# Optimization experiments

Measured on AMD Instinct MI355X. Metric: run time of the kernel, lower is better.

Reference implementation:

```python
import jax, jax.numpy as jnp
import numpy as np

B, C_IMG, H, W = 16, 512, 32, 32
C_AUD, K_LEN, N_HEADS = 512, 256, 8
HEAD_DIM = C_AUD // N_HEADS
EPS = 1e-5


def setup_inputs() -> dict:
    key = jax.random.key(0)
    ks = jax.random.split(key, 12)
    s_img = 1.0 / np.sqrt(C_IMG)
    s_aud = 1.0 / np.sqrt(C_AUD)
    return {
        "img_feat": jax.random.normal(ks[0], (B, C_IMG, H, W), jnp.float32),
        "audio_feat": jax.random.normal(ks[1], (B, K_LEN, C_AUD), jnp.float32),
        "Wq": jax.random.uniform(ks[2], (C_IMG, C_AUD), jnp.float32, -s_img, s_img),
        "bq": jnp.zeros((C_AUD,), jnp.float32),
        "Wk": jax.random.uniform(ks[3], (C_AUD, C_AUD), jnp.float32, -s_aud, s_aud),
        "bk": jnp.zeros((C_AUD,), jnp.float32),
        "Wv": jax.random.uniform(ks[4], (C_AUD, C_AUD), jnp.float32, -s_aud, s_aud),
        "bv": jnp.zeros((C_AUD,), jnp.float32),
        "Wo": jax.random.uniform(ks[5], (C_AUD, C_IMG), jnp.float32, -s_aud, s_aud),
        "bo": jnp.zeros((C_IMG,), jnp.float32),
        "gamma": jnp.ones((C_IMG,), jnp.float32),
        "beta": jnp.zeros((C_IMG,), jnp.float32),
    }


def reference(img_feat, audio_feat, Wq, bq, Wk, bk, Wv, bv, Wo, bo, gamma, beta):
    b, c, h, w = img_feat.shape
    # b c h w -> b (h w) c
    img_seq = img_feat.reshape(b, c, h * w).transpose(0, 2, 1)
    q = img_seq @ Wq + bq                      # [b, q, C_AUD]
    k = audio_feat @ Wk + bk                   # [b, k, C_AUD]
    v = audio_feat @ Wv + bv
    # split heads: b s (h d) -> b h s d
    def split(x):
        bs, s, _ = x.shape
        return x.reshape(bs, s, N_HEADS, HEAD_DIM).transpose(0, 2, 1, 3)
    qh, kh, vh = split(q), split(k), split(v)
    scale = HEAD_DIM ** -0.5
    scores = jnp.einsum('bhqd,bhkd->bhqk', qh, kh) * scale
    weights = jax.nn.softmax(scores, axis=-1)
    attn = jnp.einsum('bhqk,bhkd->bhqd', weights, vh)
    attn = attn.transpose(0, 2, 1, 3).reshape(b, h * w, C_AUD)
    proj = attn @ Wo + bo                      # [b, q, C_IMG]
    y = img_seq + proj
    mu = jnp.mean(y, axis=-1, keepdims=True)
    var = jnp.mean((y - mu) ** 2, axis=-1, keepdims=True)
    y = (y - mu) * jax.lax.rsqrt(var + EPS) * gamma + beta
    # b (h w) c -> b c h w
    return y.transpose(0, 2, 1).reshape(b, c, h, w)
```

## Files before the change

### kernel.cpp

```cpp
#include <hip/hip_runtime.h>
#include <cstddef>

#define B_SZ 16
#define HW 1024
#define CCH 512
#define K_LEN 256
#define N_HEADS 8
#define EPS 1e-5f

typedef __bf16 bf16;
typedef bf16 bf16x8 __attribute__((ext_vector_type(8)));
typedef bf16 bf16x4 __attribute__((ext_vector_type(4)));
typedef float f32x4 __attribute__((ext_vector_type(4)));

__device__ __forceinline__ void gl_lds16(const bf16* g, bf16* l) {
    __builtin_amdgcn_global_load_lds(
        (const __attribute__((address_space(1))) void*)g,
        (__attribute__((address_space(3))) void*)l, 16, 0, 0);
}

__global__ __launch_bounds__(256) void transpose_cast_img(
    const float* __restrict__ src, bf16* __restrict__ dst)
{
    const int b  = blockIdx.z;
    const int s0 = blockIdx.x * 64;
    const int c0 = blockIdx.y * 64;
    __shared__ bf16 T[64][72];
    const int tid = threadIdx.x;
    {
        const int r = tid >> 2, cs = (tid & 3) << 4;
        const float* sp = src + ((size_t)b * CCH + c0 + r) * HW + s0 + cs;
        #pragma unroll
        for (int i = 0; i < 4; ++i) {
            float4 f = *(const float4*)(sp + i * 4);
            T[r][cs + i*4 + 0] = (bf16)f.x;
            T[r][cs + i*4 + 1] = (bf16)f.y;
            T[r][cs + i*4 + 2] = (bf16)f.z;
            T[r][cs + i*4 + 3] = (bf16)f.w;
        }
    }
    __syncthreads();
    {
        const int ss = tid >> 2, ks = (tid & 3) << 4;
        bf16x8 a, b8;
        #pragma unroll
        for (int j = 0; j < 8; ++j) { a[j] = T[ks + j][ss]; b8[j] = T[ks + 8 + j][ss]; }
        bf16* dp = dst + ((size_t)b * HW + s0 + ss) * CCH + c0 + ks;
        *(bf16x8*)dp = a;
        *(bf16x8*)(dp + 8) = b8;
    }
}

__global__ __launch_bounds__(256) void transpose_cast_w(
    const float* __restrict__ Wq, const float* __restrict__ Wk,
    const float* __restrict__ Wv, const float* __restrict__ Wo,
    bf16* __restrict__ dst)
{
    const int w = blockIdx.z;
    const float* src = (w == 0) ? Wq : (w == 1) ? Wk : (w == 2) ? Wv : Wo;
    const int n0 = blockIdx.x * 64;
    const int k0 = blockIdx.y * 64;
    __shared__ bf16 T[64][72];
    const int tid = threadIdx.x;
    {
        const int r = tid >> 2, cs = (tid & 3) << 4;
        const float* sp = src + (size_t)(k0 + r) * CCH + n0 + cs;
        #pragma unroll
        for (int i = 0; i < 4; ++i) {
            float4 f = *(const float4*)(sp + i * 4);
            T[r][cs + i*4 + 0] = (bf16)f.x;
            T[r][cs + i*4 + 1] = (bf16)f.y;
            T[r][cs + i*4 + 2] = (bf16)f.z;
            T[r][cs + i*4 + 3] = (bf16)f.w;
        }
    }
    __syncthreads();
    {
        const int nn = tid >> 2, ks = (tid & 3) << 4;
        bf16x8 a, b8;
        #pragma unroll
        for (int j = 0; j < 8; ++j) { a[j] = T[ks + j][nn]; b8[j] = T[ks + 8 + j][nn]; }
        bf16* dp = dst + (size_t)w * CCH * CCH + (size_t)(n0 + nn) * CCH + k0 + ks;
        *(bf16x8*)dp = a;
        *(bf16x8*)(dp + 8) = b8;
    }
}

__global__ __launch_bounds__(256) void cast_audio(
    const float* __restrict__ src, bf16* __restrict__ dst)
{
    const size_t i = ((size_t)blockIdx.x * 256 + threadIdx.x) * 8;
    float4 a = *(const float4*)(src + i);
    float4 b = *(const float4*)(src + i + 4);
    bf16x8 o;
    o[0] = (bf16)a.x; o[1] = (bf16)a.y; o[2] = (bf16)a.z; o[3] = (bf16)a.w;
    o[4] = (bf16)b.x; o[5] = (bf16)b.y; o[6] = (bf16)b.z; o[7] = (bf16)b.w;
    *(bf16x8*)(dst + i) = o;
}

__global__ __launch_bounds__(256) void gemm_bf16_mfma(
    const bf16* __restrict__ A, const bf16* __restrict__ Bt,
    const float* __restrict__ bias, bf16* __restrict__ out)
{
    const int tid  = threadIdx.x;
    const int wave = tid >> 6, lane = tid & 63;
    const int m0 = blockIdx.x * 128;
    const int n0 = blockIdx.y * 128;
    const int l15 = lane & 15, quad = lane >> 4;
    const int wm = (wave >> 1) * 64, wn = (wave & 1) * 64;

    __shared__ bf16 As[128 * 32];
    __shared__ bf16 Bs[128 * 32];

    const int r16 = lane >> 2;
    const int ks  = (lane & 3) * 8;

    f32x4 acc[4][4];
    #pragma unroll
    for (int i = 0; i < 4; ++i)
        #pragma unroll
        for (int j = 0; j < 4; ++j)
            acc[i][j] = (f32x4){0.f, 0.f, 0.f, 0.f};

    for (int k0 = 0; k0 < 512; k0 += 32) {
        #pragma unroll
        for (int i = 0; i < 2; ++i) {
            const int c = wave * 2 + i;
            gl_lds16(A  + (size_t)(m0 + c * 16 + r16) * 512 + k0 + ks, &As[c * 512]);
            gl_lds16(Bt + (size_t)(n0 + c * 16 + r16) * 512 + k0 + ks, &Bs[c * 512]);
        }
        __syncthreads();
        bf16x8 af[4], bfr[4];
        #pragma unroll
        for (int i = 0; i < 4; ++i)
            af[i] = *(const bf16x8*)&As[(wm + i * 16 + l15) * 32 + quad * 8];
        #pragma unroll
        for (int j = 0; j < 4; ++j)
            bfr[j] = *(const bf16x8*)&Bs[(wn + j * 16 + l15) * 32 + quad * 8];
        #pragma unroll
        for (int i = 0; i < 4; ++i)
            #pragma unroll
            for (int j = 0; j < 4; ++j)
                acc[i][j] = __builtin_amdgcn_mfma_f32_16x16x32_bf16(bfr[j], af[i], acc[i][j], 0, 0, 0);
        __syncthreads();
    }

    #pragma unroll
    for (int j = 0; j < 4; ++j) {
        const int gn = n0 + wn + j * 16 + quad * 4;
        const float4 bv4 = *(const float4*)(bias + gn);
        const float bb[4] = {bv4.x, bv4.y, bv4.z, bv4.w};
        #pragma unroll
        for (int i = 0; i < 4; ++i) {
            const int gm = m0 + wm + i * 16 + l15;
            bf16x4 ov;
            #pragma unroll
            for (int r = 0; r < 4; ++r) ov[r] = (bf16)(acc[i][j][r] + bb[r]);
            *(bf16x4*)(out + (size_t)gm * 512 + gn) = ov;
        }
    }
}

__global__ __launch_bounds__(256) void gemm_kv_mfma(
    const bf16* __restrict__ A, const bf16* __restrict__ Bt,
    const float* __restrict__ bk, const float* __restrict__ bv,
    bf16* __restrict__ khout, bf16* __restrict__ vtout)
{
    const int tid  = threadIdx.x;
    const int wave = tid >> 6, lane = tid & 63;
    const int m0 = blockIdx.x * 128;
    const int n0 = blockIdx.y * 128;
    const int l15 = lane & 15, quad = lane >> 4;
    const int wm = (wave >> 1) * 64, wn = (wave & 1) * 64;

    __shared__ bf16 As[128 * 32];
    __shared__ bf16 Bs[128 * 32];

    const int r16 = lane >> 2;
    const int ks  = (lane & 3) * 8;

    f32x4 acc[4][4];
    #pragma unroll
    for (int i = 0; i < 4; ++i)
        #pragma unroll
        for (int j = 0; j < 4; ++j)
            acc[i][j] = (f32x4){0.f, 0.f, 0.f, 0.f};

    for (int k0 = 0; k0 < 512; k0 += 32) {
        #pragma unroll
        for (int i = 0; i < 2; ++i) {
            const int c = wave * 2 + i;
            gl_lds16(A  + (size_t)(m0 + c * 16 + r16) * 512 + k0 + ks, &As[c * 512]);
            gl_lds16(Bt + (size_t)(n0 + c * 16 + r16) * 512 + k0 + ks, &Bs[c * 512]);
        }
        __syncthreads();
        bf16x8 af[4], bfr[4];
        #pragma unroll
        for (int i = 0; i < 4; ++i)
            af[i] = *(const bf16x8*)&As[(wm + i * 16 + l15) * 32 + quad * 8];
        #pragma unroll
        for (int j = 0; j < 4; ++j)
            bfr[j] = *(const bf16x8*)&Bs[(wn + j * 16 + l15) * 32 + quad * 8];
        #pragma unroll
        for (int i = 0; i < 4; ++i)
            #pragma unroll
            for (int j = 0; j < 4; ++j)
                acc[i][j] = __builtin_amdgcn_mfma_f32_16x16x32_bf16(af[i], bfr[j], acc[i][j], 0, 0, 0);
        __syncthreads();
    }

    #pragma unroll
    for (int j = 0; j < 4; ++j) {
        const int gn = n0 + wn + j * 16 + l15;
        if (gn < 512) {
            const int h = gn >> 6, d = gn & 63;
            const float bias = bk[gn];
            #pragma unroll
            for (int i = 0; i < 4; ++i) {
                const int gm = m0 + wm + i * 16 + quad * 4;
                const int b = gm >> 8, key = gm & 255;
                bf16* base = khout + ((((size_t)b * N_HEADS + h) * K_LEN) + key) * 64 + d;
                #pragma unroll
                for (int r = 0; r < 4; ++r)
                    base[(size_t)r * 64] = (bf16)(acc[i][j][r] + bias);
            }
        } else {
            const int ch = gn - 512;
            const int h = ch >> 6, d = ch & 63;
            const float bias = bv[ch];
            #pragma unroll
            for (int i = 0; i < 4; ++i) {
                const int gm = m0 + wm + i * 16 + quad * 4;
                const int b = gm >> 8, key = gm & 255;
                bf16x4 pk;
                #pragma unroll
                for (int r = 0; r < 4; ++r) pk[r] = (bf16)(acc[i][j][r] + bias);
                *(bf16x4*)(vtout + (((size_t)b * N_HEADS + h) * 64 + d) * K_LEN + key) = pk;
            }
        }
    }
}

__global__ __launch_bounds__(256) void attn_mfma(
    const bf16* __restrict__ q,
    const bf16* __restrict__ kh,
    const bf16* __restrict__ vt,
    bf16* __restrict__ o)
{
    const int bh = blockIdx.x;
    const int s0 = blockIdx.y * 64;
    const int tid = threadIdx.x;
    const int wave = tid >> 6, lane = tid & 63;
    const int l15 = lane & 15, quad = lane >> 4;
    const int b = bh >> 3, h = bh & 7;

    __shared__ bf16 KsPt[18432];
    __shared__ bf16 Vs[16896];

    const bf16* khb = kh + (size_t)bh * K_LEN * 64;
    const bf16* vtb = vt + (size_t)bh * 64 * K_LEN;

    #pragma unroll
    for (int i = 0; i < 8; ++i) {
        const int chunk = tid + (i << 8);
        const int key = chunk >> 3, dseg = (chunk & 7) << 3;
        *(bf16x8*)&KsPt[key * 72 + dseg] = *(const bf16x8*)(khb + key * 64 + dseg);
        const int d = chunk >> 5, kseg = (chunk & 31) << 3;
        *(bf16x8*)&Vs[d * 264 + kseg] = *(const bf16x8*)(vtb + d * 256 + kseg);
    }
    __syncthreads();

    const int qrow = s0 + wave * 16 + l15;
    const bf16* qp = q + ((size_t)(b * HW + qrow)) * 512 + h * 64 + quad * 8;
    const bf16x8 qf0 = *(const bf16x8*)qp;
    const bf16x8 qf1 = *(const bf16x8*)(qp + 32);

    f32x4 acc[16];
    #pragma unroll
    for (int m = 0; m < 16; ++m) acc[m] = (f32x4){0.f, 0.f, 0.f, 0.f};
    #pragma unroll
    for (int m = 0; m < 16; ++m) {
        const bf16x8 a0 = *(const bf16x8*)&KsPt[(m * 16 + l15) * 72 + quad * 8];
        const bf16x8 a1 = *(const bf16x8*)&KsPt[(m * 16 + l15) * 72 + 32 + quad * 8];
        acc[m] = __builtin_amdgcn_mfma_f32_16x16x32_bf16(a0, qf0, acc[m], 0, 0, 0);
        acc[m] = __builtin_amdgcn_mfma_f32_16x16x32_bf16(a1, qf1, acc[m], 0, 0, 0);
    }

    float mx = -1e30f;
    #pragma unroll
    for (int m = 0; m < 16; ++m)
        mx = fmaxf(mx, fmaxf(fmaxf(acc[m][0], acc[m][1]), fmaxf(acc[m][2], acc[m][3])));
    mx = fmaxf(mx, __shfl_xor(mx, 16, 64));
    mx = fmaxf(mx, __shfl_xor(mx, 32, 64));

    __syncthreads();

    bf16* PtW = &KsPt[wave * 4224];
    float l_sum = 0.f;
    #pragma unroll
    for (int m = 0; m < 16; ++m) {
        bf16x4 pk;
        #pragma unroll
        for (int r = 0; r < 4; ++r) {
            const float p = __expf((acc[m][r] - mx) * 0.125f);
            l_sum += p;
            pk[r] = (bf16)p;
        }
        *(bf16x4*)&PtW[l15 * 264 + m * 16 + quad * 4] = pk;
    }
    l_sum += __shfl_xor(l_sum, 16, 64);
    l_sum += __shfl_xor(l_sum, 32, 64);
    __syncthreads();

    f32x4 oacc[4];
    #pragma unroll
    for (int m = 0; m < 4; ++m) oacc[m] = (f32x4){0.f, 0.f, 0.f, 0.f};
    #pragma unroll
    for (int s = 0; s < 8; ++s) {
        const bf16x8 pb = *(const bf16x8*)&PtW[l15 * 264 + s * 32 + quad * 8];
        #pragma unroll
        for (int m = 0; m < 4; ++m) {
            const bf16x8 va = *(const bf16x8*)&Vs[(m * 16 + l15) * 264 + s * 32 + quad * 8];
            oacc[m] = __builtin_amdgcn_mfma_f32_16x16x32_bf16(va, pb, oacc[m], 0, 0, 0);
        }
    }

    const float inv = 1.0f / l_sum;
    bf16* op = o + ((size_t)(b * HW + qrow)) * 512 + h * 64 + quad * 4;
    #pragma unroll
    for (int m = 0; m < 4; ++m) {
        bf16x4 ov;
        #pragma unroll
        for (int r = 0; r < 4; ++r) ov[r] = (bf16)(oacc[m][r] * inv);
        *(bf16x4*)&op[m * 16] = ov;
    }
}

__global__ __launch_bounds__(256) void ln_kernel(
    const bf16* __restrict__ proj, const bf16* __restrict__ imgb,
    const float* __restrict__ gamma, const float* __restrict__ beta,
    float* __restrict__ out)
{
    const int b  = blockIdx.y;
    const int s0 = blockIdx.x * 32;
    const int tid = threadIdx.x;
    const int wave = tid >> 6, lane = tid & 63;

    __shared__ float Y[32][513];

    const int cb = lane * 8;
    const float4 g0 = *(const float4*)(gamma + cb);
    const float4 g1 = *(const float4*)(gamma + cb + 4);
    const float4 b0 = *(const float4*)(beta + cb);
    const float4 b1 = *(const float4*)(beta + cb + 4);
    const float gg[8] = {g0.x, g0.y, g0.z, g0.w, g1.x, g1.y, g1.z, g1.w};
    const float bb[8] = {b0.x, b0.y, b0.z, b0.w, b1.x, b1.y, b1.z, b1.w};

    #pragma unroll
    for (int rr = 0; rr < 8; ++rr) {
        const int ss = wave * 8 + rr;
        const size_t row = (size_t)b * HW + s0 + ss;
        bf16x8 p8 = *(const bf16x8*)(proj + row * 512 + cb);
        bf16x8 i8 = *(const bf16x8*)(imgb + row * 512 + cb);
        float y[8];
        float sum = 0.f, sq = 0.f;
        #pragma unroll
        for (int j = 0; j < 8; ++j) {
            y[j] = (float)p8[j] + (float)i8[j];
            sum += y[j]; sq += y[j] * y[j];
        }
        #pragma unroll
        for (int off = 32; off > 0; off >>= 1) {
            sum += __shfl_xor(sum, off, 64);
            sq  += __shfl_xor(sq, off, 64);
        }
        const float mu = sum * (1.f / 512.f);
        const float rs = rsqrtf(sq * (1.f / 512.f) - mu * mu + EPS);
        #pragma unroll
        for (int j = 0; j < 8; ++j)
            Y[ss][cb + j] = (y[j] - mu) * rs * gg[j] + bb[j];
    }
    __syncthreads();

    #pragma unroll
    for (int it = 0; it < 16; ++it) {
        const int idx = it * 256 + tid;
        const int c = idx >> 3, sseg = (idx & 7) << 2;
        float4 o4;
        o4.x = Y[sseg + 0][c];
        o4.y = Y[sseg + 1][c];
        o4.z = Y[sseg + 2][c];
        o4.w = Y[sseg + 3][c];
        *(float4*)(out + ((size_t)b * CCH + c) * HW + s0 + sseg) = o4;
    }
}

extern "C" void kernel_launch(void* const* d_in, const int* in_sizes, int n_in,
                              void* d_out, int out_size, void* d_ws, size_t ws_size,
                              hipStream_t stream) {
    const float* img   = (const float*)d_in[0];
    const float* audio = (const float*)d_in[1];
    const float* Wq    = (const float*)d_in[2];
    const float* bq    = (const float*)d_in[3];
    const float* Wk    = (const float*)d_in[4];
    const float* bk    = (const float*)d_in[5];
    const float* Wv    = (const float*)d_in[6];
    const float* bv    = (const float*)d_in[7];
    const float* Wo    = (const float*)d_in[8];
    const float* bo    = (const float*)d_in[9];
    const float* gamma = (const float*)d_in[10];
    const float* beta  = (const float*)d_in[11];

    bf16* wsb    = (bf16*)d_ws;
    bf16* img_bf = wsb;
    bf16* aud_bf = img_bf + 8388608;
    bf16* wT     = aud_bf + 2097152;
    bf16* q_bf   = wT + 1048576;
    bf16* kh_bf  = q_bf + 8388608;
    bf16* vt_bf  = kh_bf + 2097152;
    bf16* a_bf   = vt_bf + 2097152;
    bf16* p_bf   = q_bf;

    transpose_cast_img<<<dim3(16, 8, 16), 256, 0, stream>>>(img, img_bf);
    cast_audio<<<dim3(1024), 256, 0, stream>>>(audio, aud_bf);
    transpose_cast_w<<<dim3(8, 8, 4), 256, 0, stream>>>(Wq, Wk, Wv, Wo, wT);

    gemm_bf16_mfma<<<dim3(128, 4), 256, 0, stream>>>(img_bf, wT, bq, q_bf);
    gemm_kv_mfma<<<dim3(32, 8), 256, 0, stream>>>(aud_bf, wT + 262144, bk, bv, kh_bf, vt_bf);
    attn_mfma<<<dim3(B_SZ * N_HEADS, HW / 64), 256, 0, stream>>>(q_bf, kh_bf, vt_bf, a_bf);
    gemm_bf16_mfma<<<dim3(128, 4), 256, 0, stream>>>(a_bf, wT + 3 * 262144, bo, p_bf);
    ln_kernel<<<dim3(32, 16), 256, 0, stream>>>(p_bf, img_bf, gamma, beta, (float*)d_out);
}
```

Baseline: 198.1 us.

## Fuse output projection GEMM with residual add and LayerNorm epilogue

```diff
diff --git a/kernel.cpp b/kernel.cpp
--- a/kernel.cpp
+++ b/kernel.cpp
@@ -11,6 +11,7 @@
 typedef __bf16 bf16;
 typedef bf16 bf16x8 __attribute__((ext_vector_type(8)));
 typedef bf16 bf16x4 __attribute__((ext_vector_type(4)));
+typedef bf16 bf16x2 __attribute__((ext_vector_type(2)));
 typedef float f32x4 __attribute__((ext_vector_type(4)));
 
 __device__ __forceinline__ void gl_lds16(const bf16* g, bf16* l) {
@@ -148,14 +149,13 @@
     #pragma unroll
     for (int j = 0; j < 4; ++j) {
         const int gn = n0 + wn + j * 16 + quad * 4;
-        const float4 bv4 = *(const float4*)(bias + gn);
-        const float bb[4] = {bv4.x, bv4.y, bv4.z, bv4.w};
+        const f32x4 bv4 = *(const f32x4*)(bias + gn);
         #pragma unroll
         for (int i = 0; i < 4; ++i) {
             const int gm = m0 + wm + i * 16 + l15;
             bf16x4 ov;
             #pragma unroll
-            for (int r = 0; r < 4; ++r) ov[r] = (bf16)(acc[i][j][r] + bb[r]);
+            for (int r = 0; r < 4; ++r) ov[r] = (bf16)(acc[i][j][r] + bv4[r]);
             *(bf16x4*)(out + (size_t)gm * 512 + gn) = ov;
         }
     }
@@ -336,62 +336,136 @@
     }
 }
 
-__global__ __launch_bounds__(256) void ln_kernel(
-    const bf16* __restrict__ proj, const bf16* __restrict__ imgb,
+__global__ __launch_bounds__(512) void gemm_oln(
+    const bf16* __restrict__ A,
+    const bf16* __restrict__ Wt,
+    const float* __restrict__ bo,
+    const bf16* __restrict__ imgb,
     const float* __restrict__ gamma, const float* __restrict__ beta,
     float* __restrict__ out)
 {
-    const int b  = blockIdx.y;
-    const int s0 = blockIdx.x * 32;
-    const int tid = threadIdx.x;
+    const int tid  = threadIdx.x;
     const int wave = tid >> 6, lane = tid & 63;
-
-    __shared__ float Y[32][513];
-
-    const int cb = lane * 8;
-    const float4 g0 = *(const float4*)(gamma + cb);
-    const float4 g1 = *(const float4*)(gamma + cb + 4);
-    const float4 b0 = *(const float4*)(beta + cb);
-    const float4 b1 = *(const float4*)(beta + cb + 4);
-    const float gg[8] = {g0.x, g0.y, g0.z, g0.w, g1.x, g1.y, g1.z, g1.w};
-    const float bb[8] = {b0.x, b0.y, b0.z, b0.w, b1.x, b1.y, b1.z, b1.w};
-
-    #pragma unroll
-    for (int rr = 0; rr < 8; ++rr) {
-        const int ss = wave * 8 + rr;
-        const size_t row = (size_t)b * HW + s0 + ss;
-        bf16x8 p8 = *(const bf16x8*)(proj + row * 512 + cb);
-        bf16x8 i8 = *(const bf16x8*)(imgb + row * 512 + cb);
-        float y[8];
-        float sum = 0.f, sq = 0.f;
-        #pragma unroll
-        for (int j = 0; j < 8; ++j) {
-            y[j] = (float)p8[j] + (float)i8[j];
-            sum += y[j]; sq += y[j] * y[j];
-        }
-        #pragma unroll
-        for (int off = 32; off > 0; off >>= 1) {
-            sum += __shfl_xor(sum, off, 64);
-            sq  += __shfl_xor(sq, off, 64);
-        }
-        const float mu = sum * (1.f / 512.f);
-        const float rs = rsqrtf(sq * (1.f / 512.f) - mu * mu + EPS);
-        #pragma unroll
-        for (int j = 0; j < 8; ++j)
-            Y[ss][cb + j] = (y[j] - mu) * rs * gg[j] + bb[j];
-    }
-    __syncthreads();
-
-    #pragma unroll
-    for (int it = 0; it < 16; ++it) {
-        const int idx = it * 256 + tid;
-        const int c = idx >> 3, sseg = (idx & 7) << 2;
-        float4 o4;
-        o4.x = Y[sseg + 0][c];
-        o4.y = Y[sseg + 1][c];
-        o4.z = Y[sseg + 2][c];
-        o4.w = Y[sseg + 3][c];
-        *(float4*)(out + ((size_t)b * CCH + c) * HW + s0 + sseg) = o4;
+    const int l15 = lane & 15, quad = lane >> 4;
+    const int m0 = blockIdx.x * 64;
+    const int b  = m0 >> 10, s0 = m0 & 1023;
+    const int wn = wave * 64;
+
+    __shared__ union {
+        struct { bf16 As[64 * 32]; bf16 Bs[512 * 32]; } st;
+        bf16 Ys[64 * 522];
+    } u;
+    __shared__ float rsumS[64 * 8];
+    __shared__ float rsqS[64 * 8];
+
+    const int r16 = lane >> 2;
+    const int ks  = (lane & 3) * 8;
+
+    f32x4 acc[4][4];
+    #pragma unroll
+    for (int i = 0; i < 4; ++i)
+        #pragma unroll
+        for (int j = 0; j < 4; ++j)
+            acc[i][j] = (f32x4){0.f, 0.f, 0.f, 0.f};
+
+    for (int k0 = 0; k0 < 512; k0 += 32) {
+        #pragma unroll
+        for (int t = 0; t < 4; ++t) {
+            const int cb = wave + (t << 3);
+            gl_lds16(Wt + (size_t)(cb * 16 + r16) * 512 + k0 + ks, &u.st.Bs[cb * 512]);
+        }
+        if (wave < 4)
+            gl_lds16(A + (size_t)(m0 + wave * 16 + r16) * 512 + k0 + ks, &u.st.As[wave * 512]);
+        __syncthreads();
+        bf16x8 af[4], bfr[4];
+        #pragma unroll
+        for (int i = 0; i < 4; ++i)
+            af[i] = *(const bf16x8*)&u.st.As[(i * 16 + l15) * 32 + quad * 8];
+        #pragma unroll
+        for (int j = 0; j < 4; ++j)
+            bfr[j] = *(const bf16x8*)&u.st.Bs[(wn + j * 16 + l15) * 32 + quad * 8];
+        #pragma unroll
+        for (int i = 0; i < 4; ++i)
+            #pragma unroll
+            for (int j = 0; j < 4; ++j)
+                acc[i][j] = __builtin_amdgcn_mfma_f32_16x16x32_bf16(bfr[j], af[i], acc[i][j], 0, 0, 0);
+        __syncthreads();
+    }
+
+    float rs_[4] = {0.f, 0.f, 0.f, 0.f};
+    float rq_[4] = {0.f, 0.f, 0.f, 0.f};
+    #pragma unroll
+    for (int j = 0; j < 4; ++j) {
+        const int n = wn + j * 16 + quad * 4;
+        const f32x4 bo4 = *(const f32x4*)(bo + n);
+        #pragma unroll
+        for (int i = 0; i < 4; ++i) {
+            const int lm = i * 16 + l15;
+            const bf16x4 res = *(const bf16x4*)(imgb + (size_t)(m0 + lm) * 512 + n);
+            #pragma unroll
+            for (int r = 0; r < 4; ++r) {
+                const float y = acc[i][j][r] + bo4[r] + (float)res[r];
+                acc[i][j][r] = y;
+                rs_[i] += y;
+                rq_[i] += y * y;
+            }
+        }
+    }
+    #pragma unroll
+    for (int i = 0; i < 4; ++i) {
+        rs_[i] += __shfl_xor(rs_[i], 16, 64);
+        rs_[i] += __shfl_xor(rs_[i], 32, 64);
+        rq_[i] += __shfl_xor(rq_[i], 16, 64);
+        rq_[i] += __shfl_xor(rq_[i], 32, 64);
+    }
+    if (quad == 0) {
+        #pragma unroll
+        for (int i = 0; i < 4; ++i) {
+            rsumS[(i * 16 + l15) * 8 + wave] = rs_[i];
+            rsqS[(i * 16 + l15) * 8 + wave]  = rq_[i];
+        }
+    }
+    __syncthreads();
+
+    float mu[4], rstd[4];
+    #pragma unroll
+    for (int i = 0; i < 4; ++i) {
+        const int lm = i * 16 + l15;
+        float s = 0.f, q = 0.f;
+        #pragma unroll
+        for (int w = 0; w < 8; ++w) { s += rsumS[lm * 8 + w]; q += rsqS[lm * 8 + w]; }
+        mu[i] = s * (1.f / 512.f);
+        rstd[i] = rsqrtf(q * (1.f / 512.f) - mu[i] * mu[i] + EPS);
+    }
+
+    #pragma unroll
+    for (int j = 0; j < 4; ++j) {
+        const int n = wn + j * 16 + quad * 4;
+        const f32x4 g4 = *(const f32x4*)(gamma + n);
+        const f32x4 b4 = *(const f32x4*)(beta + n);
+        #pragma unroll
+        for (int i = 0; i < 4; ++i) {
+            const int lm = i * 16 + l15;
+            float z[4];
+            #pragma unroll
+            for (int r = 0; r < 4; ++r)
+                z[r] = (acc[i][j][r] - mu[i]) * rstd[i] * g4[r] + b4[r];
+            bf16x2 z01, z23;
+            z01[0] = (bf16)z[0]; z01[1] = (bf16)z[1];
+            z23[0] = (bf16)z[2]; z23[1] = (bf16)z[3];
+            *(bf16x2*)&u.Ys[lm * 522 + n]     = z01;
+            *(bf16x2*)&u.Ys[lm * 522 + n + 2] = z23;
+        }
+    }
+    __syncthreads();
+
+    float* ob = out + (size_t)b * CCH * HW + s0 + lane;
+    #pragma unroll
+    for (int it = 0; it < 32; ++it) {
+        const int c = wn + it * 2;
+        const bf16x2 z2 = *(const bf16x2*)&u.Ys[lane * 522 + c];
+        ob[(size_t)c * HW]       = (float)z2[0];
+        ob[(size_t)(c + 1) * HW] = (float)z2[1];
     }
 }
 
@@ -419,7 +493,6 @@
     bf16* kh_bf  = q_bf + 8388608;
     bf16* vt_bf  = kh_bf + 2097152;
     bf16* a_bf   = vt_bf + 2097152;
-    bf16* p_bf   = q_bf;
 
     transpose_cast_img<<<dim3(16, 8, 16), 256, 0, stream>>>(img, img_bf);
     cast_audio<<<dim3(1024), 256, 0, stream>>>(audio, aud_bf);
@@ -428,6 +501,5 @@
     gemm_bf16_mfma<<<dim3(128, 4), 256, 0, stream>>>(img_bf, wT, bq, q_bf);
     gemm_kv_mfma<<<dim3(32, 8), 256, 0, stream>>>(aud_bf, wT + 262144, bk, bv, kh_bf, vt_bf);
     attn_mfma<<<dim3(B_SZ * N_HEADS, HW / 64), 256, 0, stream>>>(q_bf, kh_bf, vt_bf, a_bf);
-    gemm_bf16_mfma<<<dim3(128, 4), 256, 0, stream>>>(a_bf, wT + 3 * 262144, bo, p_bf);
-    ln_kernel<<<dim3(32, 16), 256, 0, stream>>>(p_bf, img_bf, gamma, beta, (float*)d_out);
-}
+    gemm_oln<<<dim3(256), 512, 0, stream>>>(a_bf, wT + 3 * 262144, bo, img_bf, gamma, beta, (float*)d_out);
+}
```

Measured after the change: 202.5 us. 1.02x slower.
